# Kernel tuning notes

Hardware: AMD Instinct MI355X
Metric: run time of the kernel (lower is better)

The kernel has to match this reference:

```python
import jax, jax.numpy as jnp
import numpy as np

N = 100000
NNZ = 3200000
K = 3

def setup_inputs() -> dict:
    key = jax.random.key(0)
    ks = jax.random.split(key, 9)
    return {
        "x": jax.random.normal(ks[0], (N, 128), dtype=jnp.float32),
        "vals": jax.random.uniform(ks[1], (NNZ,), dtype=jnp.float32) * (1.0 / 32.0),
        "W1": jax.random.normal(ks[2], (128 * K, 256), dtype=jnp.float32) * 0.05,
        "b1": jax.random.normal(ks[3], (256,), dtype=jnp.float32) * 0.05,
        "W2": jax.random.normal(ks[4], (256 * K, 64), dtype=jnp.float32) * 0.05,
        "b2": jax.random.normal(ks[5], (64,), dtype=jnp.float32) * 0.05,
        "rows": jax.random.randint(ks[6], (NNZ,), 0, N, dtype=jnp.int32),
        "cols": jax.random.randint(ks[7], (NNZ,), 0, N, dtype=jnp.int32),
        "idx": jax.random.randint(ks[8], (50000,), 0, N, dtype=jnp.int32),
    }

def _spmm(rows, cols, vals, x):
    # sparse [N,N] @ dense [N,F] via gather + segment_sum
    return jax.ops.segment_sum(vals[:, None] * x[cols], rows, num_segments=N)

def _cheb_basis(x, rows, cols, vals, k):
    # Chebyshev recurrence: T0=x, T1=L x, T_m = 2 L T_{m-1} - T_{m-2}
    xs = [x]
    if k > 1:
        x0, x1 = x, _spmm(rows, cols, vals, x)
        xs.append(x1)
        for _ in range(2, k):
            x2 = 2.0 * _spmm(rows, cols, vals, x1) - x0
            xs.append(x2)
            x0, x1 = x1, x2
    # match torch layout: [N, F, K] -> [N, F*K] (per-feature K contiguous)
    return jnp.stack(xs, axis=2).reshape(x.shape[0], -1)

def reference(x, vals, W1, b1, W2, b2, rows, cols, idx):
    h = _cheb_basis(x, rows, cols, vals, K) @ W1 + b1
    h = jax.nn.relu(h)  # dropout omitted (eval mode)
    out = _cheb_basis(h, rows, cols, vals, K) @ W2 + b2
    return out[idx]
```

## Files before the change

### kernel.cpp

```cpp
#include <hip/hip_runtime.h>
#include <hip/hip_bf16.h>

typedef __attribute__((ext_vector_type(8))) __bf16 bf16x8;
typedef __attribute__((ext_vector_type(4))) float floatx4;
typedef unsigned short ushort_t;
typedef unsigned int uint_t;

#define N_NODES 100000
#define NNZ_E   3200000
#define N_IDX   50000
#define NB_BKT  196
#define PTILE   8192
#define PBLOCKS 391

__device__ __forceinline__ float bf2f(uint_t u16) {
  union { float f; uint_t i; } v; v.i = u16 << 16; return v.f;
}
__device__ __forceinline__ unsigned short f2bf(float f) {
  union { float f; uint_t i; } v; v.f = f;
  uint_t x = v.i;
  return (unsigned short)((x + 0x7FFFu + ((x >> 16) & 1u)) >> 16);
}
__device__ __forceinline__ uint_t pk(float lo, float hi) {
  return ((uint_t)f2bf(hi) << 16) | (uint_t)f2bf(lo);
}


__global__ __launch_bounds__(256) void k_bhist(const int* __restrict__ rows,
                                               int* __restrict__ bcnt) {
  __shared__ int h[NB_BKT];
  for (int i = threadIdx.x; i < NB_BKT; i += 256) h[i] = 0;
  __syncthreads();
  int base = blockIdx.x * PTILE;
  for (int i = threadIdx.x; i < PTILE; i += 256) {
    int e = base + i;
    if (e < NNZ_E) atomicAdd(&h[rows[e] >> 9], 1);
  }
  __syncthreads();
  for (int i = threadIdx.x; i < NB_BKT; i += 256)
    if (h[i]) atomicAdd(&bcnt[i], h[i]);
}

__global__ void k_bscan(const int* __restrict__ bcnt, int* __restrict__ bbase,
                        int* __restrict__ bcur) {
  __shared__ int ts[256];
  int t = threadIdx.x;
  int v = (t < NB_BKT) ? bcnt[t] : 0;
  ts[t] = v;
  __syncthreads();
  for (int off = 1; off < 256; off <<= 1) {
    int x = ts[t];
    int a = (t >= off) ? ts[t - off] : 0;
    __syncthreads();
    ts[t] = x + a;
    __syncthreads();
  }
  if (t < NB_BKT) {
    int b = (t == 0) ? 0 : ts[t - 1];
    bbase[t] = b;
    bcur[t] = b;
  }
}

__global__ __launch_bounds__(256) void k_part(const int* __restrict__ rows,
                                              const int* __restrict__ cols,
                                              const float* __restrict__ vals,
                                              int* __restrict__ bcur,
                                              int2* __restrict__ tmp) {
  __shared__ int h[NB_BKT];
  for (int i = threadIdx.x; i < NB_BKT; i += 256) h[i] = 0;
  __syncthreads();
  int base = blockIdx.x * PTILE;
  for (int i = threadIdx.x; i < PTILE; i += 256) {
    int e = base + i;
    if (e < NNZ_E) atomicAdd(&h[rows[e] >> 9], 1);
  }
  __syncthreads();
  for (int i = threadIdx.x; i < NB_BKT; i += 256) {
    int c = h[i];
    h[i] = c ? atomicAdd(&bcur[i], c) : 0;
  }
  __syncthreads();
  for (int i = threadIdx.x; i < PTILE; i += 256) {
    int e = base + i;
    if (e < NNZ_E) {
      int rr = rows[e];
      int p = atomicAdd(&h[rr >> 9], 1);
      int2 o;
      o.x = cols[e] | ((rr & 511) << 17);
      o.y = __float_as_int(vals[e]);
      tmp[p] = o;
    }
  }
}

__global__ __launch_bounds__(512) void k_sort(const int* __restrict__ bbase,
                                              const int2* __restrict__ tmp,
                                              int2* __restrict__ edges,
                                              int* __restrict__ rowptr) {
  __shared__ int cnt[512];
  __shared__ int ts[512];
  int b = blockIdx.x, t = threadIdx.x;
  int s = bbase[b];
  int epos = (b == NB_BKT - 1) ? NNZ_E : bbase[b + 1];
  cnt[t] = 0;
  __syncthreads();
  for (int i = s + t; i < epos; i += 512)
    atomicAdd(&cnt[(tmp[i].x >> 17) & 511], 1);
  __syncthreads();
  ts[t] = cnt[t];
  __syncthreads();
  for (int off = 1; off < 512; off <<= 1) {
    int x = ts[t];
    int a = (t >= off) ? ts[t - off] : 0;
    __syncthreads();
    ts[t] = x + a;
    __syncthreads();
  }
  int pre = (t == 0) ? 0 : ts[t - 1];
  int grow = b * 512 + t;
  if (grow < N_NODES) rowptr[grow] = s + pre;
  cnt[t] = s + pre;
  __syncthreads();
  for (int i = s + t; i < epos; i += 512) {
    int2 p = tmp[i];
    int rl = (p.x >> 17) & 511;
    int pos = atomicAdd(&cnt[rl], 1);
    int2 o;
    o.x = p.x & 0x1FFFF;
    o.y = p.y;
    edges[pos] = o;
  }
  if (b == 0 && t == 0) rowptr[N_NODES] = NNZ_E;
}


__global__ __launch_bounds__(256) void k_prep(
    const float4* __restrict__ x, const float* __restrict__ W1,
    const float* __restrict__ W2, ushort4* __restrict__ xb,
    ushort_t* __restrict__ W1p, ushort_t* __restrict__ W2p) {
  int b = blockIdx.x;
  if (b < 12500) {
    int i = b * 256 + threadIdx.x;
    float4 v = x[i];
    ushort4 o;
    o.x = f2bf(v.x); o.y = f2bf(v.y); o.z = f2bf(v.z); o.w = f2bf(v.w);
    xb[i] = o;
  } else if (b < 12884) {
    int kp = b - 12500;
    int n  = threadIdx.x;
    int ch = kp >> 7;
    int f  = kp & 127;
    float v;
    if (ch == 0)      v = W1[(f*3+0)*256+n] - W1[(f*3+2)*256+n];
    else if (ch == 1) v = W1[(f*3+1)*256+n];
    else              v = 2.0f * W1[(f*3+2)*256+n];
    int kb = kp >> 5, kr = kp & 31;
    int lane = ((kr >> 3) << 4) | (n & 15);
    W1p[(((size_t)kb * 16 + (n >> 4)) * 64 + lane) * 8 + (kr & 7)] = f2bf(v);
  } else {
    int f = b - 12884;
    int c = threadIdx.x;
    if (c < 192) {
      int g = c >> 6, n = c & 63;
      float v;
      if (g == 0)      v = W2[(f*3+0)*64+n] - W2[(f*3+2)*64+n];
      else if (g == 1) v = W2[(f*3+1)*64+n];
      else             v = 2.0f * W2[(f*3+2)*64+n];
      int kb = f >> 5, kr = f & 31;
      int nb = c >> 4;
      int lane = ((kr >> 3) << 4) | (c & 15);
      W2p[(((size_t)kb * 12 + nb) * 64 + lane) * 8 + (kr & 7)] = f2bf(v);
    }
  }
}


__global__ __launch_bounds__(256) void k_spmm128(
    const int* __restrict__ rowptr, const int2* __restrict__ edges,
    const ushort_t* __restrict__ in, ushort_t* __restrict__ out, int row0) {
  int r = __builtin_amdgcn_readfirstlane(row0 + blockIdx.x * 4 + (threadIdx.x >> 6));
  int f = threadIdx.x & 63;
  int e0 = rowptr[r], e1 = rowptr[r + 1];
  float a0 = 0.f, a1 = 0.f;
  int e = e0;
  for (; e + 16 <= e1; e += 16) {
    int2 E[16];
#pragma unroll
    for (int j = 0; j < 16; ++j) E[j] = edges[e + j];
    uint_t q[16];
#pragma unroll
    for (int j = 0; j < 16; ++j)
      q[j] = *(const uint_t*)(in + (size_t)E[j].x * 128 + 2 * f);
#pragma unroll
    for (int j = 0; j < 16; ++j) {
      float v = __int_as_float(E[j].y);
      a0 = fmaf(v, bf2f(q[j] & 0xFFFFu), a0);
      a1 = fmaf(v, bf2f(q[j] >> 16), a1);
    }
  }
  for (; e + 4 <= e1; e += 4) {
    int2 E[4];
#pragma unroll
    for (int j = 0; j < 4; ++j) E[j] = edges[e + j];
    uint_t q[4];
#pragma unroll
    for (int j = 0; j < 4; ++j)
      q[j] = *(const uint_t*)(in + (size_t)E[j].x * 128 + 2 * f);
#pragma unroll
    for (int j = 0; j < 4; ++j) {
      float v = __int_as_float(E[j].y);
      a0 = fmaf(v, bf2f(q[j] & 0xFFFFu), a0);
      a1 = fmaf(v, bf2f(q[j] >> 16), a1);
    }
  }
  for (; e < e1; ++e) {
    int2 E = edges[e];
    uint_t q = *(const uint_t*)(in + (size_t)E.x * 128 + 2 * f);
    float v = __int_as_float(E.y);
    a0 = fmaf(v, bf2f(q & 0xFFFFu), a0);
    a1 = fmaf(v, bf2f(q >> 16), a1);
  }
  uint_t o = ((uint_t)f2bf(a1) << 16) | (uint_t)f2bf(a0);
  *(uint_t*)(out + (size_t)r * 128 + 2 * f) = o;
}


__global__ __launch_bounds__(256) void k_spmm64_add(
    const int* __restrict__ rowptr, const int2* __restrict__ edges,
    const ushort_t* __restrict__ p2, const ushort_t* __restrict__ p1,
    ushort_t* __restrict__ u) {
  int r = __builtin_amdgcn_readfirstlane(blockIdx.x * 4 + (threadIdx.x >> 6));
  int lane = threadIdx.x & 63;
  int half = lane >> 5, l5 = lane & 31;
  int e0 = rowptr[r], e1 = rowptr[r + 1];
  float a0 = 0.f, a1 = 0.f;
  int e = e0;
  for (; e + 16 <= e1; e += 16) {
    int2 Ea[8], Eb[8];
#pragma unroll
    for (int j = 0; j < 8; ++j) { Ea[j] = edges[e + 2*j]; Eb[j] = edges[e + 2*j + 1]; }
    uint_t q[8];
#pragma unroll
    for (int j = 0; j < 8; ++j) {
      int c = half ? Eb[j].x : Ea[j].x;
      q[j] = *(const uint_t*)(p2 + (size_t)c * 64 + 2 * l5);
    }
#pragma unroll
    for (int j = 0; j < 8; ++j) {
      float v = __int_as_float(half ? Eb[j].y : Ea[j].y);
      a0 = fmaf(v, bf2f(q[j] & 0xFFFFu), a0);
      a1 = fmaf(v, bf2f(q[j] >> 16), a1);
    }
  }
  for (; e + 2 <= e1; e += 2) {
    int2 Ea = edges[e], Eb = edges[e + 1];
    int c = half ? Eb.x : Ea.x;
    uint_t q = *(const uint_t*)(p2 + (size_t)c * 64 + 2 * l5);
    float v = __int_as_float(half ? Eb.y : Ea.y);
    a0 = fmaf(v, bf2f(q & 0xFFFFu), a0);
    a1 = fmaf(v, bf2f(q >> 16), a1);
  }
  if (e < e1) {
    int2 Ea = edges[e];
    uint_t q = *(const uint_t*)(p2 + (size_t)Ea.x * 64 + 2 * l5);
    float v = half ? 0.f : __int_as_float(Ea.y);
    a0 = fmaf(v, bf2f(q & 0xFFFFu), a0);
    a1 = fmaf(v, bf2f(q >> 16), a1);
  }
  a0 += __shfl_xor(a0, 32);
  a1 += __shfl_xor(a1, 32);
  if (half == 0) {
    uint_t pp = *(const uint_t*)(p1 + (size_t)r * 64 + 2 * l5);
    float b0 = a0 + bf2f(pp & 0xFFFFu);
    float b1 = a1 + bf2f(pp >> 16);
    *(uint_t*)(u + (size_t)r * 64 + 2 * l5) = pk(b0, b1);
  }
}


__global__ __launch_bounds__(256) void k_spmm64_idx(
    const int* __restrict__ rowptr, const int2* __restrict__ edges,
    const ushort_t* __restrict__ u, const float* __restrict__ p0,
    const int* __restrict__ idx, float* __restrict__ out) {
  int o = __builtin_amdgcn_readfirstlane(blockIdx.x * 4 + (threadIdx.x >> 6));
  int lane = threadIdx.x & 63;
  int half = lane >> 5, l5 = lane & 31;
  int r = __builtin_amdgcn_readfirstlane(idx[o]);
  int e0 = rowptr[r], e1 = rowptr[r + 1];
  float a0 = 0.f, a1 = 0.f;
  int e = e0;
  for (; e + 16 <= e1; e += 16) {
    int2 Ea[8], Eb[8];
#pragma unroll
    for (int j = 0; j < 8; ++j) { Ea[j] = edges[e + 2*j]; Eb[j] = edges[e + 2*j + 1]; }
    uint_t q[8];
#pragma unroll
    for (int j = 0; j < 8; ++j) {
      int c = half ? Eb[j].x : Ea[j].x;
      q[j] = *(const uint_t*)(u + (size_t)c * 64 + 2 * l5);
    }
#pragma unroll
    for (int j = 0; j < 8; ++j) {
      float v = __int_as_float(half ? Eb[j].y : Ea[j].y);
      a0 = fmaf(v, bf2f(q[j] & 0xFFFFu), a0);
      a1 = fmaf(v, bf2f(q[j] >> 16), a1);
    }
  }
  for (; e + 2 <= e1; e += 2) {
    int2 Ea = edges[e], Eb = edges[e + 1];
    int c = half ? Eb.x : Ea.x;
    uint_t q = *(const uint_t*)(u + (size_t)c * 64 + 2 * l5);
    float v = __int_as_float(half ? Eb.y : Ea.y);
    a0 = fmaf(v, bf2f(q & 0xFFFFu), a0);
    a1 = fmaf(v, bf2f(q >> 16), a1);
  }
  if (e < e1) {
    int2 Ea = edges[e];
    uint_t q = *(const uint_t*)(u + (size_t)Ea.x * 64 + 2 * l5);
    float v = half ? 0.f : __int_as_float(Ea.y);
    a0 = fmaf(v, bf2f(q & 0xFFFFu), a0);
    a1 = fmaf(v, bf2f(q >> 16), a1);
  }
  a0 += __shfl_xor(a0, 32);
  a1 += __shfl_xor(a1, 32);
  if (half == 0) {
    float2 b = *(const float2*)(p0 + (size_t)r * 64 + 2 * l5);
    float2 ww; ww.x = b.x + a0; ww.y = b.y + a1;
    *(float2*)(out + (size_t)o * 64 + 2 * l5) = ww;
  }
}


__global__ __launch_bounds__(256) void k_gemm1(
    const ushort_t* __restrict__ A0, const ushort_t* __restrict__ A1,
    const ushort_t* __restrict__ A2, const ushort_t* __restrict__ Bp,
    const float* __restrict__ bias, ushort_t* __restrict__ h) {
  int lane = threadIdx.x & 63;
  int ng = threadIdx.x >> 6;
  int r0 = blockIdx.x * 64;
  int mrl = lane & 15;
  int ko = (lane >> 4) << 3;
  floatx4 acc[4][4] = {};
#pragma unroll
  for (int kbg = 0; kbg < 12; ++kbg) {
    int c = kbg >> 2, kb = kbg & 3;
    const ushort_t* Asrc = (c == 0 ? A0 : c == 1 ? A1 : A2);
    bf16x8 a[4];
#pragma unroll
    for (int mi = 0; mi < 4; ++mi) {
      int mr = r0 + mi * 16 + mrl;
      if (mr > N_NODES - 1) mr = N_NODES - 1;
      a[mi] = *(const bf16x8*)(Asrc + (size_t)mr * 128 + kb * 32 + ko);
    }
    const ushort_t* Bb = Bp + (((size_t)(kbg * 16 + ng * 4)) * 64 + lane) * 8;
#pragma unroll
    for (int nt = 0; nt < 4; ++nt) {
      bf16x8 b = *(const bf16x8*)(Bb + (size_t)nt * 64 * 8);
#pragma unroll
      for (int mi = 0; mi < 4; ++mi)
        acc[mi][nt] = __builtin_amdgcn_mfma_f32_16x16x32_bf16(a[mi], b, acc[mi][nt], 0, 0, 0);
    }
  }
  int col0 = ng * 64 + (lane & 15);
  int rr0 = (lane >> 4) << 2;
#pragma unroll
  for (int nt = 0; nt < 4; ++nt) {
    int col = col0 + nt * 16;
    float bv = bias[col];
#pragma unroll
    for (int mi = 0; mi < 4; ++mi) {
      int rb = r0 + mi * 16 + rr0;
#pragma unroll
      for (int rg = 0; rg < 4; ++rg) {
        int row = rb + rg;
        if (row < N_NODES) {
          float v = acc[mi][nt][rg] + bv;
          v = v > 0.f ? v : 0.f;
          h[(size_t)row * 256 + col] = f2bf(v);
        }
      }
    }
  }
}


__global__ __launch_bounds__(256) void k_gemm2(
    const ushort_t* __restrict__ A, const ushort_t* __restrict__ Bp,
    const float* __restrict__ bias, float* __restrict__ p0,
    ushort_t* __restrict__ p1, ushort_t* __restrict__ p2) {
  int wid = (blockIdx.x * 256 + threadIdx.x) >> 6;
  int lane = threadIdx.x & 63;
  int mt4 = wid / 3, ng = wid - mt4 * 3;
  if (mt4 >= 1563) return;
  int r0 = mt4 * 64;
  int mrl = lane & 15;
  int ko = (lane >> 4) << 3;
  floatx4 acc[4][4] = {};
#pragma unroll
  for (int kb = 0; kb < 8; ++kb) {
    bf16x8 a[4];
#pragma unroll
    for (int mi = 0; mi < 4; ++mi) {
      int mr = r0 + mi * 16 + mrl;
      if (mr > N_NODES - 1) mr = N_NODES - 1;
      a[mi] = *(const bf16x8*)(A + (size_t)mr * 256 + kb * 32 + ko);
    }
    const ushort_t* Bb = Bp + (((size_t)(kb * 12 + ng * 4)) * 64 + lane) * 8;
#pragma unroll
    for (int nt = 0; nt < 4; ++nt) {
      bf16x8 b = *(const bf16x8*)(Bb + (size_t)nt * 64 * 8);
#pragma unroll
      for (int mi = 0; mi < 4; ++mi)
        acc[mi][nt] = __builtin_amdgcn_mfma_f32_16x16x32_bf16(a[mi], b, acc[mi][nt], 0, 0, 0);
    }
  }
  int c16 = lane & 15;
  int rr0 = (lane >> 4) << 2;
  if (ng == 0) {
#pragma unroll
    for (int nt = 0; nt < 4; ++nt) {
      float bv = bias[nt * 16 + c16];
#pragma unroll
      for (int mi = 0; mi < 4; ++mi) {
        int rb = r0 + mi * 16 + rr0;
#pragma unroll
        for (int rg = 0; rg < 4; ++rg) {
          int row = rb + rg;
          if (row < N_NODES)
            p0[(size_t)row * 64 + nt * 16 + c16] = acc[mi][nt][rg] + bv;
        }
      }
    }
  } else {
    ushort_t* dst = (ng == 1) ? p1 : p2;
#pragma unroll
    for (int nt = 0; nt < 4; ++nt)
#pragma unroll
      for (int mi = 0; mi < 4; ++mi) {
        int rb = r0 + mi * 16 + rr0;
#pragma unroll
        for (int rg = 0; rg < 4; ++rg) {
          int row = rb + rg;
          if (row < N_NODES)
            dst[(size_t)row * 64 + nt * 16 + c16] = f2bf(acc[mi][nt][rg]);
        }
      }
  }
}


extern "C" void kernel_launch(void* const* d_in, const int* in_sizes, int n_in,
                              void* d_out, int out_size, void* d_ws, size_t ws_size,
                              hipStream_t stream) {
  const float* x    = (const float*)d_in[0];
  const float* vals = (const float*)d_in[1];
  const float* W1   = (const float*)d_in[2];
  const float* b1   = (const float*)d_in[3];
  const float* W2   = (const float*)d_in[4];
  const float* b2   = (const float*)d_in[5];
  const int*   rows = (const int*)d_in[6];
  const int*   cols = (const int*)d_in[7];
  const int*   idx  = (const int*)d_in[8];
  float* out = (float*)d_out;

  char* w = (char*)d_ws;
  size_t off = 0;
  auto take = [&](size_t b) -> char* {
    char* p = w + off;
    off += (b + 255) & ~(size_t)255;
    return p;
  };
  int*      bcnt    = (int*)take((size_t)NB_BKT * 4);
  int*      bbase   = (int*)take((size_t)NB_BKT * 4);
  int*      bcur    = (int*)take((size_t)NB_BKT * 4);
  int*      rowptr  = (int*)take((size_t)(N_NODES + 1) * 4);
  int2*     tmp     = (int2*)take((size_t)NNZ_E * 8);
  int2*     edges   = (int2*)take((size_t)NNZ_E * 8);
  ushort_t* xb      = (ushort_t*)take((size_t)N_NODES * 128 * 2);
  ushort_t* T1a     = (ushort_t*)take((size_t)N_NODES * 128 * 2);
  ushort_t* U1      = (ushort_t*)take((size_t)N_NODES * 128 * 2);
  ushort_t* h       = (ushort_t*)take((size_t)N_NODES * 256 * 2);
  ushort_t* W1p     = (ushort_t*)take((size_t)384 * 256 * 2);
  ushort_t* W2p     = (ushort_t*)take((size_t)256 * 192 * 2);

  float*    p0 = (float*)xb;
  ushort_t* p1 = T1a;
  ushort_t* p2 = T1a + (size_t)N_NODES * 64;
  ushort_t* u  = U1;

  hipMemsetAsync(bcnt, 0, (size_t)NB_BKT * 4, stream);
  k_bhist<<<PBLOCKS, 256, 0, stream>>>(rows, bcnt);
  k_bscan<<<1, 256, 0, stream>>>(bcnt, bbase, bcur);
  k_part<<<PBLOCKS, 256, 0, stream>>>(rows, cols, vals, bcur, tmp);
  k_sort<<<NB_BKT, 512, 0, stream>>>(bbase, tmp, edges, rowptr);

  k_prep<<<13140, 256, 0, stream>>>((const float4*)x, W1, W2, (ushort4*)xb, W1p, W2p);

  k_spmm128<<<8334, 256, 0, stream>>>(rowptr, edges, xb, T1a, 0);
  k_spmm128<<<8334, 256, 0, stream>>>(rowptr, edges, xb, T1a, 33336);
  k_spmm128<<<8332, 256, 0, stream>>>(rowptr, edges, xb, T1a, 66672);
  k_spmm128<<<8334, 256, 0, stream>>>(rowptr, edges, T1a, U1, 0);
  k_spmm128<<<8334, 256, 0, stream>>>(rowptr, edges, T1a, U1, 33336);
  k_spmm128<<<8332, 256, 0, stream>>>(rowptr, edges, T1a, U1, 66672);
  k_gemm1<<<1563, 256, 0, stream>>>(xb, T1a, U1, W1p, b1, h);

  k_gemm2<<<1173, 256, 0, stream>>>(h, W2p, b2, p0, p1, p2);
  k_spmm64_add<<<N_NODES / 4, 256, 0, stream>>>(rowptr, edges, p2, p1, u);
  k_spmm64_idx<<<N_IDX / 4, 256, 0, stream>>>(rowptr, edges, u, p0, idx, out);
}
```

Before: 688.5 us.

## Stage GEMM A/B tiles in LDS via global_load_lds with swizzled layout

```diff
diff --git a/kernel.cpp b/kernel.cpp
--- a/kernel.cpp
+++ b/kernel.cpp
@@ -336,44 +336,65 @@
     const ushort_t* __restrict__ A0, const ushort_t* __restrict__ A1,
     const ushort_t* __restrict__ A2, const ushort_t* __restrict__ Bp,
     const float* __restrict__ bias, ushort_t* __restrict__ h) {
-  int lane = threadIdx.x & 63;
-  int ng = threadIdx.x >> 6;
-  int r0 = blockIdx.x * 64;
-  int mrl = lane & 15;
-  int ko = (lane >> 4) << 3;
+  __shared__ ushort_t sA[128 * 64];
+  __shared__ ushort_t sB[16 * 512];
+  int t = threadIdx.x, w = t >> 6, l = t & 63;
+  int mt = blockIdx.x >> 1, ct = blockIdx.x & 1;
+  int r0 = mt * 128;
+  int wr = w >> 1, wc = w & 1;
   floatx4 acc[4][4] = {};
-#pragma unroll
-  for (int kbg = 0; kbg < 12; ++kbg) {
-    int c = kbg >> 2, kb = kbg & 3;
-    const ushort_t* Asrc = (c == 0 ? A0 : c == 1 ? A1 : A2);
-    bf16x8 a[4];
-#pragma unroll
-    for (int mi = 0; mi < 4; ++mi) {
-      int mr = r0 + mi * 16 + mrl;
-      if (mr > N_NODES - 1) mr = N_NODES - 1;
-      a[mi] = *(const bf16x8*)(Asrc + (size_t)mr * 128 + kb * 32 + ko);
-    }
-    const ushort_t* Bb = Bp + (((size_t)(kbg * 16 + ng * 4)) * 64 + lane) * 8;
-#pragma unroll
-    for (int nt = 0; nt < 4; ++nt) {
-      bf16x8 b = *(const bf16x8*)(Bb + (size_t)nt * 64 * 8);
-#pragma unroll
-      for (int mi = 0; mi < 4; ++mi)
-        acc[mi][nt] = __builtin_amdgcn_mfma_f32_16x16x32_bf16(a[mi], b, acc[mi][nt], 0, 0, 0);
-    }
-  }
-  int col0 = ng * 64 + (lane & 15);
-  int rr0 = (lane >> 4) << 2;
+  for (int s = 0; s < 6; ++s) {
+    const ushort_t* Asrc = (s < 2) ? A0 : (s < 4) ? A1 : A2;
+    int kloc = (s & 1) << 6;
+#pragma unroll
+    for (int c = 0; c < 4; ++c) {
+      int rl = c * 32 + (t >> 3);
+      int row = r0 + rl; if (row > N_NODES - 1) row = N_NODES - 1;
+      int k8f = (t & 7) ^ (rl & 7);
+      __builtin_amdgcn_global_load_lds(
+          (const void*)(Asrc + (size_t)row * 128 + kloc + k8f * 8),
+          (void*)(sA + (c * 4 + w) * 512), 16, 0, 0);
+    }
+#pragma unroll
+    for (int i = 0; i < 4; ++i) {
+      int lc = i * 4 + w;
+      int chunkid = (s * 2 + (lc >> 3)) * 16 + ct * 8 + (lc & 7);
+      __builtin_amdgcn_global_load_lds(
+          (const void*)(Bp + (size_t)chunkid * 512 + l * 8),
+          (void*)(sB + lc * 512), 16, 0, 0);
+    }
+    __syncthreads();
+#pragma unroll
+    for (int kb = 0; kb < 2; ++kb) {
+      bf16x8 aF[4], bF[4];
+      int k8 = kb * 4 + (l >> 4);
+#pragma unroll
+      for (int mi = 0; mi < 4; ++mi) {
+        int rl = wr * 64 + mi * 16 + (l & 15);
+        aF[mi] = *(const bf16x8*)(sA + rl * 64 + ((k8 ^ (rl & 7)) * 8));
+      }
+#pragma unroll
+      for (int nt = 0; nt < 4; ++nt)
+        bF[nt] = *(const bf16x8*)(sB + ((size_t)(kb * 8 + wc * 4 + nt) * 64 + l) * 8);
+#pragma unroll
+      for (int nt = 0; nt < 4; ++nt)
+#pragma unroll
+        for (int mi = 0; mi < 4; ++mi)
+          acc[mi][nt] = __builtin_amdgcn_mfma_f32_16x16x32_bf16(aF[mi], bF[nt], acc[mi][nt], 0, 0, 0);
+    }
+    __syncthreads();
+  }
+  int col0 = ct * 128 + wc * 64 + (l & 15);
+  int rb0 = r0 + wr * 64 + ((l >> 4) << 2);
 #pragma unroll
   for (int nt = 0; nt < 4; ++nt) {
     int col = col0 + nt * 16;
     float bv = bias[col];
 #pragma unroll
     for (int mi = 0; mi < 4; ++mi) {
-      int rb = r0 + mi * 16 + rr0;
 #pragma unroll
       for (int rg = 0; rg < 4; ++rg) {
-        int row = rb + rg;
+        int row = rb0 + mi * 16 + rg;
         if (row < N_NODES) {
           float v = acc[mi][nt][rg] + bv;
           v = v > 0.f ? v : 0.f;
@@ -389,63 +410,79 @@
     const ushort_t* __restrict__ A, const ushort_t* __restrict__ Bp,
     const float* __restrict__ bias, float* __restrict__ p0,
     ushort_t* __restrict__ p1, ushort_t* __restrict__ p2) {
-  int wid = (blockIdx.x * 256 + threadIdx.x) >> 6;
-  int lane = threadIdx.x & 63;
-  int mt4 = wid / 3, ng = wid - mt4 * 3;
-  if (mt4 >= 1563) return;
-  int r0 = mt4 * 64;
-  int mrl = lane & 15;
-  int ko = (lane >> 4) << 3;
+  __shared__ ushort_t sA[256 * 64];
+  __shared__ ushort_t sB[8 * 512];
+  int t = threadIdx.x, w = t >> 6, l = t & 63;
+  int mt = blockIdx.x / 3, ct = blockIdx.x - mt * 3;
+  int r0 = mt * 256;
   floatx4 acc[4][4] = {};
-#pragma unroll
-  for (int kb = 0; kb < 8; ++kb) {
-    bf16x8 a[4];
-#pragma unroll
-    for (int mi = 0; mi < 4; ++mi) {
-      int mr = r0 + mi * 16 + mrl;
-      if (mr > N_NODES - 1) mr = N_NODES - 1;
-      a[mi] = *(const bf16x8*)(A + (size_t)mr * 256 + kb * 32 + ko);
-    }
-    const ushort_t* Bb = Bp + (((size_t)(kb * 12 + ng * 4)) * 64 + lane) * 8;
-#pragma unroll
-    for (int nt = 0; nt < 4; ++nt) {
-      bf16x8 b = *(const bf16x8*)(Bb + (size_t)nt * 64 * 8);
-#pragma unroll
-      for (int mi = 0; mi < 4; ++mi)
-        acc[mi][nt] = __builtin_amdgcn_mfma_f32_16x16x32_bf16(a[mi], b, acc[mi][nt], 0, 0, 0);
-    }
-  }
-  int c16 = lane & 15;
-  int rr0 = (lane >> 4) << 2;
-  if (ng == 0) {
+  for (int s = 0; s < 4; ++s) {
+    int kloc = s * 64;
+#pragma unroll
+    for (int c = 0; c < 8; ++c) {
+      int rl = c * 32 + (t >> 3);
+      int row = r0 + rl; if (row > N_NODES - 1) row = N_NODES - 1;
+      int k8f = (t & 7) ^ (rl & 7);
+      __builtin_amdgcn_global_load_lds(
+          (const void*)(A + (size_t)row * 256 + kloc + k8f * 8),
+          (void*)(sA + (c * 4 + w) * 512), 16, 0, 0);
+    }
+#pragma unroll
+    for (int i = 0; i < 2; ++i) {
+      int lc = i * 4 + w;
+      int chunkid = (s * 2 + (lc >> 2)) * 12 + ct * 4 + (lc & 3);
+      __builtin_amdgcn_global_load_lds(
+          (const void*)(Bp + (size_t)chunkid * 512 + l * 8),
+          (void*)(sB + lc * 512), 16, 0, 0);
+    }
+    __syncthreads();
+#pragma unroll
+    for (int kb = 0; kb < 2; ++kb) {
+      bf16x8 aF[4], bF[4];
+      int k8 = kb * 4 + (l >> 4);
+#pragma unroll
+      for (int mi = 0; mi < 4; ++mi) {
+        int rl = w * 64 + mi * 16 + (l & 15);
+        aF[mi] = *(const bf16x8*)(sA + rl * 64 + ((k8 ^ (rl & 7)) * 8));
+      }
+#pragma unroll
+      for (int nt = 0; nt < 4; ++nt)
+        bF[nt] = *(const bf16x8*)(sB + ((size_t)(kb * 4 + nt) * 64 + l) * 8);
+#pragma unroll
+      for (int nt = 0; nt < 4; ++nt)
+#pragma unroll
+        for (int mi = 0; mi < 4; ++mi)
+          acc[mi][nt] = __builtin_amdgcn_mfma_f32_16x16x32_bf16(aF[mi], bF[nt], acc[mi][nt], 0, 0, 0);
+    }
+    __syncthreads();
+  }
+  int c16 = l & 15;
+  int rb0 = r0 + w * 64 + ((l >> 4) << 2);
+  if (ct == 0) {
 #pragma unroll
     for (int nt = 0; nt < 4; ++nt) {
       float bv = bias[nt * 16 + c16];
 #pragma unroll
-      for (int mi = 0; mi < 4; ++mi) {
-        int rb = r0 + mi * 16 + rr0;
+      for (int mi = 0; mi < 4; ++mi)
 #pragma unroll
         for (int rg = 0; rg < 4; ++rg) {
-          int row = rb + rg;
+          int row = rb0 + mi * 16 + rg;
           if (row < N_NODES)
             p0[(size_t)row * 64 + nt * 16 + c16] = acc[mi][nt][rg] + bv;
         }
-      }
     }
   } else {
-    ushort_t* dst = (ng == 1) ? p1 : p2;
+    ushort_t* dst = (ct == 1) ? p1 : p2;
 #pragma unroll
     for (int nt = 0; nt < 4; ++nt)
 #pragma unroll
-      for (int mi = 0; mi < 4; ++mi) {
-        int rb = r0 + mi * 16 + rr0;
+      for (int mi = 0; mi < 4; ++mi)
 #pragma unroll
         for (int rg = 0; rg < 4; ++rg) {
-          int row = rb + rg;
+          int row = rb0 + mi * 16 + rg;
           if (row < N_NODES)
             dst[(size_t)row * 64 + nt * 16 + c16] = f2bf(acc[mi][nt][rg]);
         }
-      }
   }
 }
 
@@ -503,7 +540,7 @@
   k_spmm128<<<8334, 256, 0, stream>>>(rowptr, edges, T1a, U1, 0);
   k_spmm128<<<8334, 256, 0, stream>>>(rowptr, edges, T1a, U1, 33336);
   k_spmm128<<<8332, 256, 0, stream>>>(rowptr, edges, T1a, U1, 66672);
-  k_gemm1<<<1563, 256, 0, stream>>>(xb, T1a, U1, W1p, b1, h);
+  k_gemm1<<<1564, 256, 0, stream>>>(xb, T1a, U1, W1p, b1, h);
 
   k_gemm2<<<1173, 256, 0, stream>>>(h, W2p, b2, p0, p1, p2);
   k_spmm64_add<<<N_NODES / 4, 256, 0, stream>>>(rowptr, edges, p2, p1, u);
```

After: 666.7 us. 3.2% less time.
